# Performance work log

Measured on AMD Instinct MI355X. Metric: run time of the kernel, lower is better.

## Reference

```python
import jax, jax.numpy as jnp
import numpy as np

B = 100000   # batch of nodes
K = 10       # sampled neighbours per node
N = 1000000  # total nodes in feature table
D = 128      # feature dim


def setup_inputs() -> dict:
    key = jax.random.key(0)
    k1, k2, k3 = jax.random.split(key, 3)
    nodes = jax.random.randint(k1, (B,), 0, N, dtype=jnp.int64)
    neighbours = jax.random.randint(k2, (B, K), 0, N, dtype=jnp.int64)
    features = jax.random.normal(k3, (N, D), dtype=jnp.float32)
    return {"nodes": nodes, "neighbours": neighbours, "features": features}


def reference(nodes, neighbours, features):
    # Neighborhood = sampled neighbours union self node -> [B, K+1]
    neigh_idx = jnp.concatenate([neighbours, nodes[:, None]], axis=1)
    # Gather features: [B, K+1, D] (irregular memory-bound gather)
    gathered = features[neigh_idx]
    # Row-normalized mask matmul == mean over the neighborhood axis
    return gathered.mean(axis=1)  # [B, D]
```

## Files before the change

kernel.cpp:

```cpp
#include <hip/hip_runtime.h>


#define KNEIGH 10
#define DDIM 128

typedef float v4f __attribute__((ext_vector_type(4)));

__global__ __launch_bounds__(256) void MeanAggregator_36386962932386_kernel(
    const int* __restrict__ nodes,
    const int* __restrict__ neighbours,
    const float* __restrict__ features,
    float* __restrict__ out,
    int B)
{
    const int wave = blockIdx.x * 4 + (threadIdx.x >> 6);
    const int lane = threadIdx.x & 63;
    const int half = lane >> 5;
    const int hl   = lane & 31;
    const unsigned hb = (unsigned)hl * 16u;

    const int npairs = (B + 1) >> 1;
    const int nwaves = gridDim.x * 4;

    int pair = wave;
    if (pair >= npairs) return;

    int idx[KNEIGH + 1];
    int node;

    {
        node = pair * 2 + half;
        const int n = node < B ? node : 0;
        const int2* p2 = (const int2*)((const char*)neighbours + (unsigned)n * (KNEIGH * 4));
#pragma unroll
        for (int j = 0; j < KNEIGH / 2; ++j) {
            const int2 t = p2[j];
            idx[2 * j]     = t.x;
            idx[2 * j + 1] = t.y;
        }
        idx[KNEIGH] = nodes[n];
    }

    while (true) {
        v4f v[KNEIGH + 1];
#pragma unroll
        for (int j = 0; j < KNEIGH + 1; ++j) {
            const unsigned off = (unsigned)idx[j] * (DDIM * 4) + hb;
            v[j] = *(const v4f*)((const char*)features + off);
        }

        const int next = pair + nwaves;
        const bool have_next = next < npairs;
        int nidx[KNEIGH + 1];
        int nnode = 0;
        if (have_next) {
            nnode = next * 2 + half;
            const int n = nnode < B ? nnode : 0;
            const int2* p2 = (const int2*)((const char*)neighbours + (unsigned)n * (KNEIGH * 4));
#pragma unroll
            for (int j = 0; j < KNEIGH / 2; ++j) {
                const int2 t = p2[j];
                nidx[2 * j]     = t.x;
                nidx[2 * j + 1] = t.y;
            }
            nidx[KNEIGH] = nodes[n];
        }

        v4f acc = v[0];
#pragma unroll
        for (int j = 1; j < KNEIGH + 1; ++j) acc += v[j];
        acc *= (1.0f / (KNEIGH + 1));

        if (node < B) {
            const unsigned ooff = (unsigned)node * (DDIM * 4) + hb;
            __builtin_nontemporal_store(acc, (v4f*)((char*)out + ooff));
        }

        if (!have_next) break;
        pair = next;
        node = nnode;
#pragma unroll
        for (int j = 0; j < KNEIGH + 1; ++j) idx[j] = nidx[j];
    }
}

extern "C" void kernel_launch(void* const* d_in, const int* in_sizes, int n_in,
                              void* d_out, int out_size, void* d_ws, size_t ws_size,
                              hipStream_t stream)
{
    const int* nodes      = (const int*)d_in[0];
    const int* neighbours = (const int*)d_in[1];
    const float* features = (const float*)d_in[2];
    float* out            = (float*)d_out;

    const int B = in_sizes[0];
    const int npairs = (B + 1) / 2;
    int blocks = (npairs + 3) / 4;
    if (blocks > 2048) blocks = 2048;

    MeanAggregator_36386962932386_kernel<<<blocks, 256, 0, stream>>>(
        nodes, neighbours, features, out, B);
}
```

Before: 654.1 us.

## Split gather into two feature-table halves with streaming cache warm-up passes

Replaces the single persistent gather kernel with two passes, each covering half of the feature table. Before each pass, a warm kernel streams that half (about 256MB) to pull it into the last-level cache. The gather then reads only indices inside the current half, substituting a dummy row for the others. The second pass adds its sum to the first pass's partial result in the output and divides by the neighbour count. The aim is to turn random DRAM gathers into cache hits, at the cost of reading the full 512MB table sequentially, launching four kernels, issuing every gather load twice, and an extra output read-modify-write.

After: 745.1 us. +13.9%, slower.

```diff
diff --git a/kernel.cpp b/kernel.cpp
--- a/kernel.cpp
+++ b/kernel.cpp
@@ -6,12 +6,26 @@
 
 typedef float v4f __attribute__((ext_vector_type(4)));
 
+__global__ __launch_bounds__(256) void MeanAggregator_warm_kernel(
+    const float* __restrict__ features, long long lo_elem, long long n_elem,
+    float* __restrict__ sink)
+{
+    const long long tid    = (long long)blockIdx.x * 256 + threadIdx.x;
+    const long long stride = (long long)gridDim.x * 256;
+    const v4f* p = (const v4f*)(features + lo_elem);
+    const long long nvec = n_elem >> 2;
+    v4f acc = {0.f, 0.f, 0.f, 0.f};
+    for (long long i = tid; i < nvec; i += stride) acc += p[i];
+    if (acc.x == 1234567.25f && acc.y == -7654321.125f)
+        sink[threadIdx.x] = acc.z + acc.w;
+}
+
 __global__ __launch_bounds__(256) void MeanAggregator_36386962932386_kernel(
     const int* __restrict__ nodes,
     const int* __restrict__ neighbours,
     const float* __restrict__ features,
     float* __restrict__ out,
-    int B)
+    int B, int lo, int hi, int final_pass)
 {
     const int wave = blockIdx.x * 4 + (threadIdx.x >> 6);
     const int lane = threadIdx.x & 63;
@@ -20,18 +34,13 @@
     const unsigned hb = (unsigned)hl * 16u;
 
     const int npairs = (B + 1) >> 1;
-    const int nwaves = gridDim.x * 4;
-
-    int pair = wave;
-    if (pair >= npairs) return;
+    if (wave >= npairs) return;
+    const int node = wave * 2 + half;
+    const int n = node < B ? node : 0;
 
     int idx[KNEIGH + 1];
-    int node;
-
     {
-        node = pair * 2 + half;
-        const int n = node < B ? node : 0;
-        const int2* p2 = (const int2*)((const char*)neighbours + (unsigned)n * (KNEIGH * 4));
+        const int2* p2 = (const int2*)neighbours + n * (KNEIGH / 2);
 #pragma unroll
         for (int j = 0; j < KNEIGH / 2; ++j) {
             const int2 t = p2[j];
@@ -41,46 +50,31 @@
         idx[KNEIGH] = nodes[n];
     }
 
-    while (true) {
-        v4f v[KNEIGH + 1];
+    v4f v[KNEIGH + 1];
+    bool m[KNEIGH + 1];
 #pragma unroll
-        for (int j = 0; j < KNEIGH + 1; ++j) {
-            const unsigned off = (unsigned)idx[j] * (DDIM * 4) + hb;
-            v[j] = *(const v4f*)((const char*)features + off);
+    for (int j = 0; j <= KNEIGH; ++j) {
+        const int ix = idx[j];
+        const bool in = (ix >= lo) & (ix < hi);
+        const int e = in ? ix : lo;
+        m[j] = in;
+        v[j] = *(const v4f*)((const char*)features + (unsigned)e * (DDIM * 4) + hb);
+    }
+
+    const v4f z = {0.f, 0.f, 0.f, 0.f};
+    v4f acc = z;
+#pragma unroll
+    for (int j = 0; j <= KNEIGH; ++j) acc += (m[j] ? v[j] : z);
+
+    if (node < B) {
+        char* op = (char*)out + (unsigned)node * (DDIM * 4) + hb;
+        if (final_pass) {
+            v4f prev = __builtin_nontemporal_load((const v4f*)op);
+            v4f r = (acc + prev) * (1.0f / (KNEIGH + 1));
+            __builtin_nontemporal_store(r, (v4f*)op);
+        } else {
+            __builtin_nontemporal_store(acc, (v4f*)op);
         }
-
-        const int next = pair + nwaves;
-        const bool have_next = next < npairs;
-        int nidx[KNEIGH + 1];
-        int nnode = 0;
-        if (have_next) {
-            nnode = next * 2 + half;
-            const int n = nnode < B ? nnode : 0;
-            const int2* p2 = (const int2*)((const char*)neighbours + (unsigned)n * (KNEIGH * 4));
-#pragma unroll
-            for (int j = 0; j < KNEIGH / 2; ++j) {
-                const int2 t = p2[j];
-                nidx[2 * j]     = t.x;
-                nidx[2 * j + 1] = t.y;
-            }
-            nidx[KNEIGH] = nodes[n];
-        }
-
-        v4f acc = v[0];
-#pragma unroll
-        for (int j = 1; j < KNEIGH + 1; ++j) acc += v[j];
-        acc *= (1.0f / (KNEIGH + 1));
-
-        if (node < B) {
-            const unsigned ooff = (unsigned)node * (DDIM * 4) + hb;
-            __builtin_nontemporal_store(acc, (v4f*)((char*)out + ooff));
-        }
-
-        if (!have_next) break;
-        pair = next;
-        node = nnode;
-#pragma unroll
-        for (int j = 0; j < KNEIGH + 1; ++j) idx[j] = nidx[j];
     }
 }
 
@@ -94,10 +88,24 @@
     float* out            = (float*)d_out;
 
     const int B = in_sizes[0];
-    const int npairs = (B + 1) / 2;
-    int blocks = (npairs + 3) / 4;
-    if (blocks > 2048) blocks = 2048;
+    long long featElems = in_sizes[2];
+    int N = (int)(featElems / DDIM);
+    if (N <= 0) N = 1000000;
+    const int H = N / 2;
 
-    MeanAggregator_36386962932386_kernel<<<blocks, 256, 0, stream>>>(
-        nodes, neighbours, features, out, B);
+    const int npairs  = (B + 1) / 2;
+    const int gblocks = (npairs + 3) / 4;
+    const int wblocks = 2048;
+
+    float* sink = ws_size ? (float*)d_ws : out;
+
+    MeanAggregator_warm_kernel<<<wblocks, 256, 0, stream>>>(
+        features, 0LL, (long long)H * DDIM, sink);
+    MeanAggregator_36386962932386_kernel<<<gblocks, 256, 0, stream>>>(
+        nodes, neighbours, features, out, B, 0, H, 0);
+
+    MeanAggregator_warm_kernel<<<wblocks, 256, 0, stream>>>(
+        features, (long long)H * DDIM, (long long)(N - H) * DDIM, sink);
+    MeanAggregator_36386962932386_kernel<<<gblocks, 256, 0, stream>>>(
+        nodes, neighbours, features, out, B, H, N, 1);
 }
```
